# Kernel optimization log

Hardware: AMD Instinct MI355X
Metric: run time of the kernel (lower is better)

The kernel has to match this reference:

```python
import jax, jax.numpy as jnp
import numpy as np

QUERY_DIM, FEAT_DIM, HID_DIM, OUT_DIM = 512, 2048, 512, 512
B, L, S, T = 8, 128, 100, 100


def setup_inputs() -> dict:
    key = jax.random.key(0)
    ks = jax.random.split(key, 9)
    d = {
        "query": jax.random.normal(ks[0], (B, L, QUERY_DIM), jnp.float32),
        "src": jax.random.normal(ks[1], (B, S, FEAT_DIM), jnp.float32),
        "trg": jax.random.normal(ks[2], (B, T, FEAT_DIM), jnp.float32),
        # params (LinearAct == Linear + identity act); src/trg projections share weights
        "Wq": jax.random.normal(ks[3], (QUERY_DIM, HID_DIM), jnp.float32) / np.sqrt(QUERY_DIM),
        "bq": jnp.zeros((HID_DIM,), jnp.float32),
        "Ws": jax.random.normal(ks[4], (FEAT_DIM, HID_DIM), jnp.float32) / np.sqrt(FEAT_DIM),
        "bs": jnp.zeros((HID_DIM,), jnp.float32),
        "Wo": jax.random.normal(ks[5], (HID_DIM + QUERY_DIM, OUT_DIM), jnp.float32) / np.sqrt(HID_DIM + QUERY_DIM),
        "bo": jnp.zeros((OUT_DIM,), jnp.float32),
    }
    return d


def reference(query, src, trg, Wq, bq, Ws, bs, Wo, bo):
    b, l, _ = query.shape
    s = src.shape[1]
    t = trg.shape[1]
    q = query @ Wq + bq          # b,l,k
    s_key = src @ Ws + bs        # b,s,k
    t_key = trg @ Ws + bs        # b,t,k
    hid = q.shape[-1]
    # score[b,l,s,t] = q . (s_key - t_key)/sqrt(2) / sqrt(hid) -- decomposed, no b,s,t,k tensor
    qs = jnp.einsum('blk,bsk->bls', q, s_key)
    qt = jnp.einsum('blk,btk->blt', q, t_key)
    score = (qs[:, :, :, None] - qt[:, :, None, :]) / jnp.sqrt(jnp.asarray(2.0 * hid, q.dtype))
    w = jax.nn.softmax(score.reshape(b, l, s * t), axis=-1).reshape(b, l, s, t)
    # ctx = sum_{s,t} w * (s_key - t_key)/sqrt(2), decomposed via marginals
    ws = w.sum(axis=3)           # b,l,s
    wt = w.sum(axis=2)           # b,l,t
    ctx = (jnp.einsum('bls,bsk->blk', ws, s_key) - jnp.einsum('blt,btk->blk', wt, t_key)) / jnp.sqrt(jnp.asarray(2.0, q.dtype))
    x = jnp.concatenate([query, ctx], axis=-1) @ Wo + bo
    return x
```

## Files before the change

kernel.cpp:

```cpp
#include <hip/hip_runtime.h>
#include <math.h>


typedef __attribute__((ext_vector_type(8))) short s16x8;
typedef __attribute__((ext_vector_type(4))) float f32x4;

__device__ __forceinline__ unsigned short f2bf(float f) {
    unsigned int u = __float_as_uint(f);
    return (unsigned short)((u + 0x7fffu + ((u >> 16) & 1u)) >> 16);
}

__global__ __launch_bounds__(256) void k_prep(
    const float* __restrict__ query, const float* __restrict__ src,
    const float* __restrict__ trg, const float* __restrict__ Wq,
    const float* __restrict__ Ws, const float* __restrict__ Wo,
    const float* __restrict__ bs, unsigned short* __restrict__ qbf,
    unsigned short* __restrict__ aout, unsigned short* __restrict__ abf,
    unsigned short* __restrict__ WqT, unsigned short* __restrict__ WsT,
    unsigned short* __restrict__ WoT, float* __restrict__ keys) {
    __shared__ float tile[32][33];
    const int bid = blockIdx.x, t = threadIdx.x;

    if (bid < 3712) {
        const int idx = bid * 256 + t;
        if (idx < 131072) {
            float4 v = *(const float4*)(query + (size_t)idx * 4);
            ushort4 o = make_ushort4(f2bf(v.x), f2bf(v.y), f2bf(v.z), f2bf(v.w));
            *(ushort4*)(qbf + (size_t)idx * 4) = o;
            const int flat = idx * 4, m = flat >> 9, c = flat & 511;
            *(ushort4*)(aout + (size_t)m * 1024 + c) = o;
        } else if (idx < 540672) {
            const int i = idx - 131072;
            float4 v = *(const float4*)(src + (size_t)i * 4);
            *(ushort4*)(abf + (size_t)i * 4) =
                make_ushort4(f2bf(v.x), f2bf(v.y), f2bf(v.z), f2bf(v.w));
        } else {
            const int i = idx - 540672;
            float4 v = *(const float4*)(trg + (size_t)i * 4);
            *(ushort4*)(abf + 1638400 + (size_t)i * 4) =
                make_ushort4(f2bf(v.x), f2bf(v.y), f2bf(v.z), f2bf(v.w));
        }
    } else if (bid < 5504) {
        const int id = bid - 3712;
        const float* W; unsigned short* O; int K, tk, tn;
        if (id < 256)       { W = Wq; O = WqT; K = 512;  tk = id >> 4;          tn = id & 15; }
        else if (id < 1280) { W = Ws; O = WsT; K = 2048; tk = (id - 256) >> 4;  tn = (id - 256) & 15; }
        else                { W = Wo; O = WoT; K = 1024; tk = (id - 1280) >> 4; tn = (id - 1280) & 15; }
        const int row = t >> 3, c4 = (t & 7) * 4;
        float4 v = *(const float4*)(W + (size_t)(tk * 32 + row) * 512 + tn * 32 + c4);
        tile[row][c4 + 0] = v.x; tile[row][c4 + 1] = v.y;
        tile[row][c4 + 2] = v.z; tile[row][c4 + 3] = v.w;
        __syncthreads();
        ushort4 o = make_ushort4(f2bf(tile[c4 + 0][row]), f2bf(tile[c4 + 1][row]),
                                 f2bf(tile[c4 + 2][row]), f2bf(tile[c4 + 3][row]));
        *(ushort4*)(O + (size_t)(tn * 32 + row) * K + tk * 32 + c4) = o;
    } else {
        const int i = (bid - 5504) * 256 + t;
        const int f = i * 4;
        *(float4*)(keys + f) = *(const float4*)(bs + (f & 511));
    }
}


__device__ __forceinline__ void gemm64_atomic(
    const unsigned short* __restrict__ A, const unsigned short* __restrict__ BT,
    float* __restrict__ C, int m0, int n0, int K, int N, int kbase, int kiters,
    unsigned short* As, unsigned short* Bs) {
    const int t = threadIdx.x;
    const int lane = t & 63, wid = t >> 6;
    const int wm = (wid & 1) * 32, wn = (wid >> 1) * 32;
    const int lr = lane & 15, lq = lane >> 4;

    f32x4 acc[2][2] = {};
    for (int it = 0; it < kiters; it++) {
        const int kt = kbase + it * 64;
        __syncthreads();
#pragma unroll
        for (int i = 0; i < 2; i++) {
            const int idx = i * 256 + t, r = idx >> 3, c = idx & 7;
            *(s16x8*)&As[r * 72 + c * 8] =
                *(const s16x8*)(A + (size_t)(m0 + r) * K + kt + c * 8);
            *(s16x8*)&Bs[r * 72 + c * 8] =
                *(const s16x8*)(BT + (size_t)(n0 + r) * K + kt + c * 8);
        }
        __syncthreads();
#pragma unroll
        for (int s = 0; s < 2; s++) {
            s16x8 a0 = *(const s16x8*)&As[(wm + lr) * 72      + s * 32 + lq * 8];
            s16x8 a1 = *(const s16x8*)&As[(wm + 16 + lr) * 72 + s * 32 + lq * 8];
            s16x8 b0 = *(const s16x8*)&Bs[(wn + lr) * 72      + s * 32 + lq * 8];
            s16x8 b1 = *(const s16x8*)&Bs[(wn + 16 + lr) * 72 + s * 32 + lq * 8];
            acc[0][0] = __builtin_amdgcn_mfma_f32_16x16x32_bf16(a0, b0, acc[0][0], 0, 0, 0);
            acc[0][1] = __builtin_amdgcn_mfma_f32_16x16x32_bf16(a0, b1, acc[0][1], 0, 0, 0);
            acc[1][0] = __builtin_amdgcn_mfma_f32_16x16x32_bf16(a1, b0, acc[1][0], 0, 0, 0);
            acc[1][1] = __builtin_amdgcn_mfma_f32_16x16x32_bf16(a1, b1, acc[1][1], 0, 0, 0);
        }
    }
#pragma unroll
    for (int i = 0; i < 2; i++)
#pragma unroll
        for (int j = 0; j < 2; j++) {
            const int col = n0 + wn + j * 16 + lr;
            const int row = m0 + wm + i * 16 + lq * 4;
#pragma unroll
            for (int r = 0; r < 4; r++)
                unsafeAtomicAdd(&C[(size_t)(row + r) * N + col], acc[i][j][r]);
        }
}

__device__ __forceinline__ void gemm32(
    const unsigned short* __restrict__ A, const unsigned short* __restrict__ BT,
    const float* __restrict__ bias, float* __restrict__ C,
    int m0, int n0, int K, int N, int kiters,
    unsigned short* As, unsigned short* Bs) {
    const int t = threadIdx.x;
    const int lane = t & 63, wid = t >> 6;
    const int wm = (wid & 1) * 16, wn = (wid >> 1) * 32;
    const int lr = lane & 15, lq = lane >> 4;

    f32x4 acc[2] = {};
    for (int it = 0; it < kiters; it++) {
        const int kt = it * 64;
        __syncthreads();
        {
            const int r = t >> 3, c = t & 7;
            *(s16x8*)&As[r * 72 + c * 8] =
                *(const s16x8*)(A + (size_t)(m0 + r) * K + kt + c * 8);
        }
#pragma unroll
        for (int i = 0; i < 2; i++) {
            const int idx = i * 256 + t, r = idx >> 3, c = idx & 7;
            *(s16x8*)&Bs[r * 72 + c * 8] =
                *(const s16x8*)(BT + (size_t)(n0 + r) * K + kt + c * 8);
        }
        __syncthreads();
#pragma unroll
        for (int s = 0; s < 2; s++) {
            s16x8 a0 = *(const s16x8*)&As[(wm + lr) * 72      + s * 32 + lq * 8];
            s16x8 b0 = *(const s16x8*)&Bs[(wn + lr) * 72      + s * 32 + lq * 8];
            s16x8 b1 = *(const s16x8*)&Bs[(wn + 16 + lr) * 72 + s * 32 + lq * 8];
            acc[0] = __builtin_amdgcn_mfma_f32_16x16x32_bf16(a0, b0, acc[0], 0, 0, 0);
            acc[1] = __builtin_amdgcn_mfma_f32_16x16x32_bf16(a0, b1, acc[1], 0, 0, 0);
        }
    }
#pragma unroll
    for (int j = 0; j < 2; j++) {
        const int col = n0 + wn + j * 16 + lr;
        const int row = m0 + wm + lq * 4;
        const float bv = bias[col];
#pragma unroll
        for (int r = 0; r < 4; r++)
            C[(size_t)(row + r) * N + col] = acc[j][r] + bv;
    }
}

__global__ __launch_bounds__(256) void k_stageB(
    const unsigned short* __restrict__ qbf, const unsigned short* __restrict__ abf,
    const unsigned short* __restrict__ WqT, const unsigned short* __restrict__ WsT,
    const float* __restrict__ bq, float* __restrict__ q, float* __restrict__ keys) {
    __shared__ __align__(16) unsigned short As[64 * 72];
    __shared__ __align__(16) unsigned short Bs[64 * 72];
    const int bid = blockIdx.x;
    if (bid < 800) {
        const int c = bid / 200, rem = bid % 200;
        const int mt = rem >> 3, nt = rem & 7;
        gemm64_atomic(abf, WsT, keys, mt * 64, nt * 64, 2048, 512, c * 512, 8, As, Bs);
    } else {
        const int r = bid - 800;
        const int mt = r >> 3, nt = r & 7;
        gemm32(qbf, WqT, bq, q, mt * 32, nt * 64, 512, 512, 8, As, Bs);
    }
}

__global__ __launch_bounds__(256) void k_out(
    const unsigned short* __restrict__ aout, const unsigned short* __restrict__ WoT,
    const float* __restrict__ bo, float* __restrict__ out) {
    __shared__ __align__(16) unsigned short As[64 * 72];
    __shared__ __align__(16) unsigned short Bs[64 * 72];
    gemm32(aout, WoT, bo, out, blockIdx.y * 32, blockIdx.x * 64, 1024, 512, 16, As, Bs);
}

__global__ __launch_bounds__(256) void k_scores(
    const float* __restrict__ q, const float* __restrict__ keys,
    float* __restrict__ wsT, float* __restrict__ wtT) {
    __shared__ __align__(16) float qsh[512];
    __shared__ float sc[200];

    const int t = threadIdx.x;
    const int row = blockIdx.x;
    const int b = row >> 7, l = row & 127;

    if (t < 128)
        *(float4*)&qsh[t * 4] = *(const float4*)(q + (size_t)row * 512 + t * 4);
    __syncthreads();

    const int wave = t >> 6, lane = t & 63;
    const float4* qp = (const float4*)qsh;
    const float4 qv1 = qp[lane], qv2 = qp[lane + 64];

    for (int idx = wave; idx < 200; idx += 4) {
        const int kr = (idx < 100) ? (b * 100 + idx)
                                   : (800 + b * 100 + (idx - 100));
        const float4* kp = (const float4*)(keys + (size_t)kr * 512);
        const float4 kv1 = kp[lane], kv2 = kp[lane + 64];
        float d = kv1.x * qv1.x + kv1.y * qv1.y + kv1.z * qv1.z + kv1.w * qv1.w
                + kv2.x * qv2.x + kv2.y * qv2.y + kv2.z * qv2.z + kv2.w * qv2.w;
#pragma unroll
        for (int off = 32; off > 0; off >>= 1) d += __shfl_down(d, off);
        if (lane == 0)
            sc[idx] = ((idx < 100) ? d : -d) * (1.0f / 32.0f);
    }
    __syncthreads();

    if (wave < 2) {
        const float* sp = sc + wave * 100;
        const bool hi = (lane + 64) < 100;
        const float v0 = sp[lane];
        const float v1 = hi ? sp[lane + 64] : -INFINITY;
        float mx = fmaxf(v0, v1);
#pragma unroll
        for (int off = 32; off > 0; off >>= 1) mx = fmaxf(mx, __shfl_xor(mx, off));
        const float e0 = __expf(v0 - mx);
        const float e1 = hi ? __expf(v1 - mx) : 0.f;
        float s = e0 + e1;
#pragma unroll
        for (int off = 32; off > 0; off >>= 1) s += __shfl_xor(s, off);
        const float inv = 1.f / s;
        float* op = (wave == 0) ? wsT : wtT;
        op[(b * 100 + lane) * 128 + l] = e0 * inv;
        if (hi) op[(b * 100 + lane + 64) * 128 + l] = e1 * inv;
    }
}

__global__ __launch_bounds__(256) void k_ctx(
    const float* __restrict__ wsT, const float* __restrict__ wtT,
    const float* __restrict__ keys, unsigned short* __restrict__ aout) {
    __shared__ float As[40][64];
    __shared__ float Bs[40][32];

    const int t = threadIdx.x;
    const int b = blockIdx.y;
    const int n0 = blockIdx.x * 32;
    const int l0 = blockIdx.z * 64;
    const int tx = t & 7, ty = t >> 3;

    float acc[2][4] = {};

    for (int c5 = 0; c5 < 5; c5++) {
        const int kbase = c5 * 40;
        __syncthreads();
#pragma unroll
        for (int e = 0; e < 10; e++) {
            const int idx = t + e * 256;
            const int k = idx >> 6, j = idx & 63;
            const int kk = kbase + k;
            As[k][j] = (kk < 100) ? wsT[(b * 100 + kk) * 128 + l0 + j]
                                  : wtT[(b * 100 + (kk - 100)) * 128 + l0 + j];
        }
#pragma unroll
        for (int e = 0; e < 5; e++) {
            const int idx = t + e * 256;
            const int k = idx >> 5, j = idx & 31;
            const int kk = kbase + k;
            Bs[k][j] = (kk < 100)
                ?  keys[(size_t)(b * 100 + kk) * 512 + n0 + j]
                : -keys[(size_t)(800 + b * 100 + (kk - 100)) * 512 + n0 + j];
        }
        __syncthreads();
#pragma unroll 8
        for (int k = 0; k < 40; k++) {
            float ar0 = As[k][ty * 2], ar1 = As[k][ty * 2 + 1];
            float br[4];
            *(float4*)br = *(const float4*)&Bs[k][tx * 4];
#pragma unroll
            for (int j = 0; j < 4; j++) {
                acc[0][j] = fmaf(ar0, br[j], acc[0][j]);
                acc[1][j] = fmaf(ar1, br[j], acc[1][j]);
            }
        }
    }

    const float s2 = 0.70710678118654752f;
#pragma unroll
    for (int i = 0; i < 2; i++) {
        const int m = b * 128 + l0 + ty * 2 + i;
        ushort4 o = make_ushort4(f2bf(acc[i][0] * s2), f2bf(acc[i][1] * s2),
                                 f2bf(acc[i][2] * s2), f2bf(acc[i][3] * s2));
        *(ushort4*)(aout + (size_t)m * 1024 + 512 + n0 + tx * 4) = o;
    }
}


extern "C" void kernel_launch(void* const* d_in, const int* in_sizes, int n_in,
                              void* d_out, int out_size, void* d_ws, size_t ws_size,
                              hipStream_t stream) {
    const float* query = (const float*)d_in[0];
    const float* src   = (const float*)d_in[1];
    const float* trg   = (const float*)d_in[2];
    const float* Wq    = (const float*)d_in[3];
    const float* bq    = (const float*)d_in[4];
    const float* Ws    = (const float*)d_in[5];
    const float* bs    = (const float*)d_in[6];
    const float* Wo    = (const float*)d_in[7];
    const float* bo    = (const float*)d_in[8];
    float* out = (float*)d_out;

    float* q    = (float*)d_ws;
    float* keys = q    + 524288;
    float* wsT  = keys + 819200;
    float* wtT  = wsT  + 102400;
    unsigned short* qbf = (unsigned short*)(wtT + 102400);
    unsigned short* abf = qbf + 524288;
    unsigned short* aout= abf + 3276800;
    unsigned short* wqt = aout + 1048576;
    unsigned short* wst = wqt  + 262144;
    unsigned short* wot = wst  + 1048576;

    k_prep<<<6304, 256, 0, stream>>>(query, src, trg, Wq, Ws, Wo, bs,
                                     qbf, aout, abf, wqt, wst, wot, keys);
    k_stageB<<<1056, 256, 0, stream>>>(qbf, abf, wqt, wst, bq, q, keys);
    k_scores<<<1024, 256, 0, stream>>>(q, keys, wsT, wtT);
    k_ctx<<<dim3(16, 8, 2), 256, 0, stream>>>(wsT, wtT, keys, aout);
    k_out<<<dim3(8, 32), 256, 0, stream>>>(aout, wot, bo, out);
}
```

Baseline: 158.8 us.

## Fuse all stages into one persistent kernel with grid-wide barriers

Replaces the five separate kernel launches with one persistent kernel of 512 blocks that loops over virtual blocks for each stage. Stages are separated by software grid barriers built on an atomic counter, which is reset by a memset before each launch. The output GEMM now splits K in two and accumulates atomically into an output buffer pre-filled with the bias. The aim is to remove launch gaps and tail effects between stages. In exchange it relies on every block being co-resident, adds spin-wait barrier cost, and adds contention from the atomic accumulation.

```diff
diff --git a/kernel.cpp b/kernel.cpp
--- a/kernel.cpp
+++ b/kernel.cpp
@@ -4,63 +4,33 @@
 
 typedef __attribute__((ext_vector_type(8))) short s16x8;
 typedef __attribute__((ext_vector_type(4))) float f32x4;
+
+#define NBLK 512u
 
 __device__ __forceinline__ unsigned short f2bf(float f) {
     unsigned int u = __float_as_uint(f);
     return (unsigned short)((u + 0x7fffu + ((u >> 16) & 1u)) >> 16);
 }
 
-__global__ __launch_bounds__(256) void k_prep(
-    const float* __restrict__ query, const float* __restrict__ src,
-    const float* __restrict__ trg, const float* __restrict__ Wq,
-    const float* __restrict__ Ws, const float* __restrict__ Wo,
-    const float* __restrict__ bs, unsigned short* __restrict__ qbf,
-    unsigned short* __restrict__ aout, unsigned short* __restrict__ abf,
-    unsigned short* __restrict__ WqT, unsigned short* __restrict__ WsT,
-    unsigned short* __restrict__ WoT, float* __restrict__ keys) {
-    __shared__ float tile[32][33];
-    const int bid = blockIdx.x, t = threadIdx.x;
-
-    if (bid < 3712) {
-        const int idx = bid * 256 + t;
-        if (idx < 131072) {
-            float4 v = *(const float4*)(query + (size_t)idx * 4);
-            ushort4 o = make_ushort4(f2bf(v.x), f2bf(v.y), f2bf(v.z), f2bf(v.w));
-            *(ushort4*)(qbf + (size_t)idx * 4) = o;
-            const int flat = idx * 4, m = flat >> 9, c = flat & 511;
-            *(ushort4*)(aout + (size_t)m * 1024 + c) = o;
-        } else if (idx < 540672) {
-            const int i = idx - 131072;
-            float4 v = *(const float4*)(src + (size_t)i * 4);
-            *(ushort4*)(abf + (size_t)i * 4) =
-                make_ushort4(f2bf(v.x), f2bf(v.y), f2bf(v.z), f2bf(v.w));
-        } else {
-            const int i = idx - 540672;
-            float4 v = *(const float4*)(trg + (size_t)i * 4);
-            *(ushort4*)(abf + 1638400 + (size_t)i * 4) =
-                make_ushort4(f2bf(v.x), f2bf(v.y), f2bf(v.z), f2bf(v.w));
-        }
-    } else if (bid < 5504) {
-        const int id = bid - 3712;
-        const float* W; unsigned short* O; int K, tk, tn;
-        if (id < 256)       { W = Wq; O = WqT; K = 512;  tk = id >> 4;          tn = id & 15; }
-        else if (id < 1280) { W = Ws; O = WsT; K = 2048; tk = (id - 256) >> 4;  tn = (id - 256) & 15; }
-        else                { W = Wo; O = WoT; K = 1024; tk = (id - 1280) >> 4; tn = (id - 1280) & 15; }
-        const int row = t >> 3, c4 = (t & 7) * 4;
-        float4 v = *(const float4*)(W + (size_t)(tk * 32 + row) * 512 + tn * 32 + c4);
-        tile[row][c4 + 0] = v.x; tile[row][c4 + 1] = v.y;
-        tile[row][c4 + 2] = v.z; tile[row][c4 + 3] = v.w;
-        __syncthreads();
-        ushort4 o = make_ushort4(f2bf(tile[c4 + 0][row]), f2bf(tile[c4 + 1][row]),
-                                 f2bf(tile[c4 + 2][row]), f2bf(tile[c4 + 3][row]));
-        *(ushort4*)(O + (size_t)(tn * 32 + row) * K + tk * 32 + c4) = o;
-    } else {
-        const int i = (bid - 5504) * 256 + t;
-        const int f = i * 4;
-        *(float4*)(keys + f) = *(const float4*)(bs + (f & 511));
-    }
-}
-
+__device__ __forceinline__ void gbar(unsigned* cnt) {
+    __syncthreads();
+    if (threadIdx.x == 0) {
+        __hip_atomic_fetch_add(cnt, 1u, __ATOMIC_RELEASE,
+                               __HIP_MEMORY_SCOPE_AGENT);
+        unsigned spins = 0;
+        while (__hip_atomic_load(cnt, __ATOMIC_ACQUIRE,
+                                 __HIP_MEMORY_SCOPE_AGENT) < NBLK &&
+               ++spins < (8u << 20)) { }
+    }
+    __syncthreads();
+}
+
+struct MegaArgs {
+    const float *query, *src, *trg, *Wq, *bq, *Ws, *bs, *Wo, *bo;
+    unsigned short *qbf, *abf, *aout, *wqt, *wst, *wot;
+    float *q, *keys, *wsT, *wtT, *out;
+    unsigned *bar;
+};
 
 __device__ __forceinline__ void gemm64_atomic(
     const unsigned short* __restrict__ A, const unsigned short* __restrict__ BT,
@@ -108,10 +78,11 @@
         }
 }
 
+template <bool ATOMIC>
 __device__ __forceinline__ void gemm32(
     const unsigned short* __restrict__ A, const unsigned short* __restrict__ BT,
     const float* __restrict__ bias, float* __restrict__ C,
-    int m0, int n0, int K, int N, int kiters,
+    int m0, int n0, int K, int N, int kbase, int kiters,
     unsigned short* As, unsigned short* Bs) {
     const int t = threadIdx.x;
     const int lane = t & 63, wid = t >> 6;
@@ -120,7 +91,7 @@
 
     f32x4 acc[2] = {};
     for (int it = 0; it < kiters; it++) {
-        const int kt = it * 64;
+        const int kt = kbase + it * 64;
         __syncthreads();
         {
             const int r = t >> 3, c = t & 7;
@@ -147,163 +118,215 @@
     for (int j = 0; j < 2; j++) {
         const int col = n0 + wn + j * 16 + lr;
         const int row = m0 + wm + lq * 4;
-        const float bv = bias[col];
-#pragma unroll
-        for (int r = 0; r < 4; r++)
-            C[(size_t)(row + r) * N + col] = acc[j][r] + bv;
-    }
-}
-
-__global__ __launch_bounds__(256) void k_stageB(
-    const unsigned short* __restrict__ qbf, const unsigned short* __restrict__ abf,
-    const unsigned short* __restrict__ WqT, const unsigned short* __restrict__ WsT,
-    const float* __restrict__ bq, float* __restrict__ q, float* __restrict__ keys) {
-    __shared__ __align__(16) unsigned short As[64 * 72];
-    __shared__ __align__(16) unsigned short Bs[64 * 72];
-    const int bid = blockIdx.x;
-    if (bid < 800) {
-        const int c = bid / 200, rem = bid % 200;
+        if (ATOMIC) {
+#pragma unroll
+            for (int r = 0; r < 4; r++)
+                unsafeAtomicAdd(&C[(size_t)(row + r) * N + col], acc[j][r]);
+        } else {
+            const float bv = bias[col];
+#pragma unroll
+            for (int r = 0; r < 4; r++)
+                C[(size_t)(row + r) * N + col] = acc[j][r] + bv;
+        }
+    }
+}
+
+__global__ __launch_bounds__(256, 2) void k_mega(MegaArgs p) {
+    __shared__ __align__(16) unsigned char smem[18432];
+    unsigned short* As = (unsigned short*)smem;
+    unsigned short* Bs = (unsigned short*)(smem + 9216);
+    const int t = threadIdx.x;
+    const int nb = gridDim.x;
+
+    for (int vb = blockIdx.x; vb < 6816; vb += nb) {
+        if (vb < 3712) {
+            const int idx = vb * 256 + t;
+            if (idx < 131072) {
+                float4 v = *(const float4*)(p.query + (size_t)idx * 4);
+                ushort4 o = make_ushort4(f2bf(v.x), f2bf(v.y), f2bf(v.z), f2bf(v.w));
+                *(ushort4*)(p.qbf + (size_t)idx * 4) = o;
+                const int flat = idx * 4, m = flat >> 9, c = flat & 511;
+                *(ushort4*)(p.aout + (size_t)m * 1024 + c) = o;
+            } else if (idx < 540672) {
+                const int i = idx - 131072;
+                float4 v = *(const float4*)(p.src + (size_t)i * 4);
+                *(ushort4*)(p.abf + (size_t)i * 4) =
+                    make_ushort4(f2bf(v.x), f2bf(v.y), f2bf(v.z), f2bf(v.w));
+            } else {
+                const int i = idx - 540672;
+                float4 v = *(const float4*)(p.trg + (size_t)i * 4);
+                *(ushort4*)(p.abf + 1638400 + (size_t)i * 4) =
+                    make_ushort4(f2bf(v.x), f2bf(v.y), f2bf(v.z), f2bf(v.w));
+            }
+        } else if (vb < 5504) {
+            float* tile = (float*)smem;
+            const int id = vb - 3712;
+            const float* W; unsigned short* O; int K, tk, tn;
+            if (id < 256)       { W = p.Wq; O = p.wqt; K = 512;  tk = id >> 4;          tn = id & 15; }
+            else if (id < 1280) { W = p.Ws; O = p.wst; K = 2048; tk = (id - 256) >> 4;  tn = (id - 256) & 15; }
+            else                { W = p.Wo; O = p.wot; K = 1024; tk = (id - 1280) >> 4; tn = (id - 1280) & 15; }
+            const int row = t >> 3, c4 = (t & 7) * 4;
+            float4 v = *(const float4*)(W + (size_t)(tk * 32 + row) * 512 + tn * 32 + c4);
+            tile[row * 33 + c4 + 0] = v.x; tile[row * 33 + c4 + 1] = v.y;
+            tile[row * 33 + c4 + 2] = v.z; tile[row * 33 + c4 + 3] = v.w;
+            __syncthreads();
+            ushort4 o = make_ushort4(
+                f2bf(tile[(c4 + 0) * 33 + row]), f2bf(tile[(c4 + 1) * 33 + row]),
+                f2bf(tile[(c4 + 2) * 33 + row]), f2bf(tile[(c4 + 3) * 33 + row]));
+            *(ushort4*)(O + (size_t)(tn * 32 + row) * K + tk * 32 + c4) = o;
+            __syncthreads();
+        } else if (vb < 6304) {
+            const int f = ((vb - 5504) * 256 + t) * 4;
+            *(float4*)(p.keys + f) = *(const float4*)(p.bs + (f & 511));
+        } else {
+            const int f = ((vb - 6304) * 256 + t) * 4;
+            *(float4*)(p.out + f) = *(const float4*)(p.bo + (f & 511));
+        }
+    }
+    gbar(p.bar + 0);
+
+    for (int vb = blockIdx.x; vb < 1056; vb += nb) {
+        if (vb < 800) {
+            const int c = vb / 200, rem = vb % 200;
+            const int mt = rem >> 3, nt = rem & 7;
+            gemm64_atomic(p.abf, p.wst, p.keys, mt * 64, nt * 64, 2048, 512,
+                          c * 512, 8, As, Bs);
+        } else {
+            const int r = vb - 800;
+            const int mt = r >> 3, nt = r & 7;
+            gemm32<false>(p.qbf, p.wqt, p.bq, p.q, mt * 32, nt * 64, 512, 512,
+                          0, 8, As, Bs);
+        }
+    }
+    gbar(p.bar + 16);
+
+    {
+        float* qsh = (float*)smem;
+        float* sc  = (float*)(smem + 2048);
+        const int wave = t >> 6, lane = t & 63;
+        for (int vb = blockIdx.x; vb < 1024; vb += nb) {
+            const int b = vb >> 7, l = vb & 127;
+            if (t < 128)
+                *(float4*)&qsh[t * 4] =
+                    *(const float4*)(p.q + (size_t)vb * 512 + t * 4);
+            __syncthreads();
+            const float4* qp = (const float4*)qsh;
+            const float4 qv1 = qp[lane], qv2 = qp[lane + 64];
+
+            for (int idx = wave; idx < 200; idx += 4) {
+                const int kr = (idx < 100) ? (b * 100 + idx)
+                                           : (800 + b * 100 + (idx - 100));
+                const float4* kp = (const float4*)(p.keys + (size_t)kr * 512);
+                const float4 kv1 = kp[lane], kv2 = kp[lane + 64];
+                float d = kv1.x * qv1.x + kv1.y * qv1.y + kv1.z * qv1.z + kv1.w * qv1.w
+                        + kv2.x * qv2.x + kv2.y * qv2.y + kv2.z * qv2.z + kv2.w * qv2.w;
+#pragma unroll
+                for (int off = 32; off > 0; off >>= 1) d += __shfl_down(d, off);
+                if (lane == 0)
+                    sc[idx] = ((idx < 100) ? d : -d) * (1.0f / 32.0f);
+            }
+            __syncthreads();
+
+            if (wave < 2) {
+                const float* sp = sc + wave * 100;
+                const bool hi = (lane + 64) < 100;
+                const float v0 = sp[lane];
+                const float v1 = hi ? sp[lane + 64] : -INFINITY;
+                float mx = fmaxf(v0, v1);
+#pragma unroll
+                for (int off = 32; off > 0; off >>= 1) mx = fmaxf(mx, __shfl_xor(mx, off));
+                const float e0 = __expf(v0 - mx);
+                const float e1 = hi ? __expf(v1 - mx) : 0.f;
+                float s = e0 + e1;
+#pragma unroll
+                for (int off = 32; off > 0; off >>= 1) s += __shfl_xor(s, off);
+                const float inv = 1.f / s;
+                float* op = (wave == 0) ? p.wsT : p.wtT;
+                op[(b * 100 + lane) * 128 + l] = e0 * inv;
+                if (hi) op[(b * 100 + lane + 64) * 128 + l] = e1 * inv;
+            }
+            __syncthreads();
+        }
+    }
+    gbar(p.bar + 32);
+
+    {
+        float* cAs = (float*)smem;
+        float* cBs = (float*)(smem + 10240);
+        const int tx = t & 7, ty = t >> 3;
+        for (int vb = blockIdx.x; vb < 256; vb += nb) {
+            const int n0 = (vb & 15) * 32;
+            const int b  = (vb >> 4) & 7;
+            const int l0 = (vb >> 7) * 64;
+            float acc[2][4] = {};
+            for (int c5 = 0; c5 < 5; c5++) {
+                const int kbase = c5 * 40;
+                __syncthreads();
+#pragma unroll
+                for (int e = 0; e < 10; e++) {
+                    const int idx = t + e * 256;
+                    const int k = idx >> 6, j = idx & 63;
+                    const int kk = kbase + k;
+                    cAs[k * 64 + j] = (kk < 100)
+                        ? p.wsT[(b * 100 + kk) * 128 + l0 + j]
+                        : p.wtT[(b * 100 + (kk - 100)) * 128 + l0 + j];
+                }
+#pragma unroll
+                for (int e = 0; e < 5; e++) {
+                    const int idx = t + e * 256;
+                    const int k = idx >> 5, j = idx & 31;
+                    const int kk = kbase + k;
+                    cBs[k * 32 + j] = (kk < 100)
+                        ?  p.keys[(size_t)(b * 100 + kk) * 512 + n0 + j]
+                        : -p.keys[(size_t)(800 + b * 100 + (kk - 100)) * 512 + n0 + j];
+                }
+                __syncthreads();
+#pragma unroll 8
+                for (int k = 0; k < 40; k++) {
+                    float ar0 = cAs[k * 64 + ty * 2], ar1 = cAs[k * 64 + ty * 2 + 1];
+                    float br[4];
+                    *(float4*)br = *(const float4*)&cBs[k * 32 + tx * 4];
+#pragma unroll
+                    for (int j = 0; j < 4; j++) {
+                        acc[0][j] = fmaf(ar0, br[j], acc[0][j]);
+                        acc[1][j] = fmaf(ar1, br[j], acc[1][j]);
+                    }
+                }
+            }
+            const float s2 = 0.70710678118654752f;
+#pragma unroll
+            for (int i = 0; i < 2; i++) {
+                const int m = b * 128 + l0 + ty * 2 + i;
+                ushort4 o = make_ushort4(f2bf(acc[i][0] * s2), f2bf(acc[i][1] * s2),
+                                         f2bf(acc[i][2] * s2), f2bf(acc[i][3] * s2));
+                *(ushort4*)(p.aout + (size_t)m * 1024 + 512 + n0 + tx * 4) = o;
+            }
+        }
+    }
+    gbar(p.bar + 48);
+
+    for (int vb = blockIdx.x; vb < 512; vb += nb) {
+        const int c = vb >> 8, rem = vb & 255;
         const int mt = rem >> 3, nt = rem & 7;
-        gemm64_atomic(abf, WsT, keys, mt * 64, nt * 64, 2048, 512, c * 512, 8, As, Bs);
-    } else {
-        const int r = bid - 800;
-        const int mt = r >> 3, nt = r & 7;
-        gemm32(qbf, WqT, bq, q, mt * 32, nt * 64, 512, 512, 8, As, Bs);
-    }
-}
-
-__global__ __launch_bounds__(256) void k_out(
-    const unsigned short* __restrict__ aout, const unsigned short* __restrict__ WoT,
-    const float* __restrict__ bo, float* __restrict__ out) {
-    __shared__ __align__(16) unsigned short As[64 * 72];
-    __shared__ __align__(16) unsigned short Bs[64 * 72];
-    gemm32(aout, WoT, bo, out, blockIdx.y * 32, blockIdx.x * 64, 1024, 512, 16, As, Bs);
-}
-
-__global__ __launch_bounds__(256) void k_scores(
-    const float* __restrict__ q, const float* __restrict__ keys,
-    float* __restrict__ wsT, float* __restrict__ wtT) {
-    __shared__ __align__(16) float qsh[512];
-    __shared__ float sc[200];
-
-    const int t = threadIdx.x;
-    const int row = blockIdx.x;
-    const int b = row >> 7, l = row & 127;
-
-    if (t < 128)
-        *(float4*)&qsh[t * 4] = *(const float4*)(q + (size_t)row * 512 + t * 4);
-    __syncthreads();
-
-    const int wave = t >> 6, lane = t & 63;
-    const float4* qp = (const float4*)qsh;
-    const float4 qv1 = qp[lane], qv2 = qp[lane + 64];
-
-    for (int idx = wave; idx < 200; idx += 4) {
-        const int kr = (idx < 100) ? (b * 100 + idx)
-                                   : (800 + b * 100 + (idx - 100));
-        const float4* kp = (const float4*)(keys + (size_t)kr * 512);
-        const float4 kv1 = kp[lane], kv2 = kp[lane + 64];
-        float d = kv1.x * qv1.x + kv1.y * qv1.y + kv1.z * qv1.z + kv1.w * qv1.w
-                + kv2.x * qv2.x + kv2.y * qv2.y + kv2.z * qv2.z + kv2.w * qv2.w;
-#pragma unroll
-        for (int off = 32; off > 0; off >>= 1) d += __shfl_down(d, off);
-        if (lane == 0)
-            sc[idx] = ((idx < 100) ? d : -d) * (1.0f / 32.0f);
-    }
-    __syncthreads();
-
-    if (wave < 2) {
-        const float* sp = sc + wave * 100;
-        const bool hi = (lane + 64) < 100;
-        const float v0 = sp[lane];
-        const float v1 = hi ? sp[lane + 64] : -INFINITY;
-        float mx = fmaxf(v0, v1);
-#pragma unroll
-        for (int off = 32; off > 0; off >>= 1) mx = fmaxf(mx, __shfl_xor(mx, off));
-        const float e0 = __expf(v0 - mx);
-        const float e1 = hi ? __expf(v1 - mx) : 0.f;
-        float s = e0 + e1;
-#pragma unroll
-        for (int off = 32; off > 0; off >>= 1) s += __shfl_xor(s, off);
-        const float inv = 1.f / s;
-        float* op = (wave == 0) ? wsT : wtT;
-        op[(b * 100 + lane) * 128 + l] = e0 * inv;
-        if (hi) op[(b * 100 + lane + 64) * 128 + l] = e1 * inv;
-    }
-}
-
-__global__ __launch_bounds__(256) void k_ctx(
-    const float* __restrict__ wsT, const float* __restrict__ wtT,
-    const float* __restrict__ keys, unsigned short* __restrict__ aout) {
-    __shared__ float As[40][64];
-    __shared__ float Bs[40][32];
-
-    const int t = threadIdx.x;
-    const int b = blockIdx.y;
-    const int n0 = blockIdx.x * 32;
-    const int l0 = blockIdx.z * 64;
-    const int tx = t & 7, ty = t >> 3;
-
-    float acc[2][4] = {};
-
-    for (int c5 = 0; c5 < 5; c5++) {
-        const int kbase = c5 * 40;
-        __syncthreads();
-#pragma unroll
-        for (int e = 0; e < 10; e++) {
-            const int idx = t + e * 256;
-            const int k = idx >> 6, j = idx & 63;
-            const int kk = kbase + k;
-            As[k][j] = (kk < 100) ? wsT[(b * 100 + kk) * 128 + l0 + j]
-                                  : wtT[(b * 100 + (kk - 100)) * 128 + l0 + j];
-        }
-#pragma unroll
-        for (int e = 0; e < 5; e++) {
-            const int idx = t + e * 256;
-            const int k = idx >> 5, j = idx & 31;
-            const int kk = kbase + k;
-            Bs[k][j] = (kk < 100)
-                ?  keys[(size_t)(b * 100 + kk) * 512 + n0 + j]
-                : -keys[(size_t)(800 + b * 100 + (kk - 100)) * 512 + n0 + j];
-        }
-        __syncthreads();
-#pragma unroll 8
-        for (int k = 0; k < 40; k++) {
-            float ar0 = As[k][ty * 2], ar1 = As[k][ty * 2 + 1];
-            float br[4];
-            *(float4*)br = *(const float4*)&Bs[k][tx * 4];
-#pragma unroll
-            for (int j = 0; j < 4; j++) {
-                acc[0][j] = fmaf(ar0, br[j], acc[0][j]);
-                acc[1][j] = fmaf(ar1, br[j], acc[1][j]);
-            }
-        }
-    }
-
-    const float s2 = 0.70710678118654752f;
-#pragma unroll
-    for (int i = 0; i < 2; i++) {
-        const int m = b * 128 + l0 + ty * 2 + i;
-        ushort4 o = make_ushort4(f2bf(acc[i][0] * s2), f2bf(acc[i][1] * s2),
-                                 f2bf(acc[i][2] * s2), f2bf(acc[i][3] * s2));
-        *(ushort4*)(aout + (size_t)m * 1024 + 512 + n0 + tx * 4) = o;
-    }
-}
-
+        gemm32<true>(p.aout, p.wot, nullptr, p.out, mt * 32, nt * 64, 1024, 512,
+                     c * 512, 8, As, Bs);
+    }
+}
 
 extern "C" void kernel_launch(void* const* d_in, const int* in_sizes, int n_in,
                               void* d_out, int out_size, void* d_ws, size_t ws_size,
                               hipStream_t stream) {
-    const float* query = (const float*)d_in[0];
-    const float* src   = (const float*)d_in[1];
-    const float* trg   = (const float*)d_in[2];
-    const float* Wq    = (const float*)d_in[3];
-    const float* bq    = (const float*)d_in[4];
-    const float* Ws    = (const float*)d_in[5];
-    const float* bs    = (const float*)d_in[6];
-    const float* Wo    = (const float*)d_in[7];
-    const float* bo    = (const float*)d_in[8];
-    float* out = (float*)d_out;
+    MegaArgs a;
+    a.query = (const float*)d_in[0];
+    a.src   = (const float*)d_in[1];
+    a.trg   = (const float*)d_in[2];
+    a.Wq    = (const float*)d_in[3];
+    a.bq    = (const float*)d_in[4];
+    a.Ws    = (const float*)d_in[5];
+    a.bs    = (const float*)d_in[6];
+    a.Wo    = (const float*)d_in[7];
+    a.bo    = (const float*)d_in[8];
+    a.out   = (float*)d_out;
 
     float* q    = (float*)d_ws;
     float* keys = q    + 524288;
@@ -315,11 +338,13 @@
     unsigned short* wqt = aout + 1048576;
     unsigned short* wst = wqt  + 262144;
     unsigned short* wot = wst  + 1048576;
-
-    k_prep<<<6304, 256, 0, stream>>>(query, src, trg, Wq, Ws, Wo, bs,
-                                     qbf, aout, abf, wqt, wst, wot, keys);
-    k_stageB<<<1056, 256, 0, stream>>>(qbf, abf, wqt, wst, bq, q, keys);
-    k_scores<<<1024, 256, 0, stream>>>(q, keys, wsT, wtT);
-    k_ctx<<<dim3(16, 8, 2), 256, 0, stream>>>(wsT, wtT, keys, aout);
-    k_out<<<dim3(8, 32), 256, 0, stream>>>(aout, wot, bo, out);
-}
+    unsigned* bar = (unsigned*)(wot + 524288);
+
+    a.q = q; a.keys = keys; a.wsT = wsT; a.wtT = wtT;
+    a.qbf = qbf; a.abf = abf; a.aout = aout;
+    a.wqt = wqt; a.wst = wst; a.wot = wot;
+    a.bar = bar;
+
+    hipMemsetAsync(bar, 0, 256, stream);
+    k_mega<<<dim3(NBLK), dim3(256), 0, stream>>>(a);
+}
```

Measured after the change: 394.2 us. 148% more time.

## Prefetch GEMM tiles into registers, split-K output GEMM, and shrink ctx tiles

Applied to the files above, without the earlier changes.

The GEMM helpers now load the next K tile into registers while the current tile is being computed from LDS, a register-level double buffer that hides global latency. The output GEMM is split along K into two halves that accumulate atomically into an output pre-filled with the bias by the prep kernel. The ctx kernel uses 32-row tiles with register prefetch, so it launches twice as many blocks. These changes raise parallelism and overlap at the cost of atomics, extra register pressure, and a bias pre-fill pass over the output.

```diff
diff --git a/kernel.cpp b/kernel.cpp
--- a/kernel.cpp
+++ b/kernel.cpp
@@ -14,10 +14,11 @@
     const float* __restrict__ query, const float* __restrict__ src,
     const float* __restrict__ trg, const float* __restrict__ Wq,
     const float* __restrict__ Ws, const float* __restrict__ Wo,
-    const float* __restrict__ bs, unsigned short* __restrict__ qbf,
-    unsigned short* __restrict__ aout, unsigned short* __restrict__ abf,
-    unsigned short* __restrict__ WqT, unsigned short* __restrict__ WsT,
-    unsigned short* __restrict__ WoT, float* __restrict__ keys) {
+    const float* __restrict__ bs, const float* __restrict__ bo,
+    unsigned short* __restrict__ qbf, unsigned short* __restrict__ aout,
+    unsigned short* __restrict__ abf, unsigned short* __restrict__ WqT,
+    unsigned short* __restrict__ WsT, unsigned short* __restrict__ WoT,
+    float* __restrict__ keys, float* __restrict__ out) {
     __shared__ float tile[32][33];
     const int bid = blockIdx.x, t = threadIdx.x;
 
@@ -54,10 +55,12 @@
         ushort4 o = make_ushort4(f2bf(tile[c4 + 0][row]), f2bf(tile[c4 + 1][row]),
                                  f2bf(tile[c4 + 2][row]), f2bf(tile[c4 + 3][row]));
         *(ushort4*)(O + (size_t)(tn * 32 + row) * K + tk * 32 + c4) = o;
+    } else if (bid < 6304) {
+        const int f = ((bid - 5504) * 256 + t) * 4;
+        *(float4*)(keys + f) = *(const float4*)(bs + (f & 511));
     } else {
-        const int i = (bid - 5504) * 256 + t;
-        const int f = i * 4;
-        *(float4*)(keys + f) = *(const float4*)(bs + (f & 511));
+        const int f = ((bid - 6304) * 256 + t) * 4;
+        *(float4*)(out + f) = *(const float4*)(bo + (f & 511));
     }
 }
 
@@ -70,20 +73,25 @@
     const int lane = t & 63, wid = t >> 6;
     const int wm = (wid & 1) * 32, wn = (wid >> 1) * 32;
     const int lr = lane & 15, lq = lane >> 4;
+    const int r = t >> 3, c8 = (t & 7) * 8;
+
+    s16x8 ra0, ra1, rb0, rb1;
+#define LD64(kt)                                                           \
+    ra0 = *(const s16x8*)(A  + (size_t)(m0 + r)      * K + (kt) + c8);     \
+    ra1 = *(const s16x8*)(A  + (size_t)(m0 + r + 32) * K + (kt) + c8);     \
+    rb0 = *(const s16x8*)(BT + (size_t)(n0 + r)      * K + (kt) + c8);     \
+    rb1 = *(const s16x8*)(BT + (size_t)(n0 + r + 32) * K + (kt) + c8);
 
     f32x4 acc[2][2] = {};
+    LD64(kbase);
     for (int it = 0; it < kiters; it++) {
-        const int kt = kbase + it * 64;
-        __syncthreads();
-#pragma unroll
-        for (int i = 0; i < 2; i++) {
-            const int idx = i * 256 + t, r = idx >> 3, c = idx & 7;
-            *(s16x8*)&As[r * 72 + c * 8] =
-                *(const s16x8*)(A + (size_t)(m0 + r) * K + kt + c * 8);
-            *(s16x8*)&Bs[r * 72 + c * 8] =
-                *(const s16x8*)(BT + (size_t)(n0 + r) * K + kt + c * 8);
-        }
-        __syncthreads();
+        __syncthreads();
+        *(s16x8*)&As[r * 72 + c8]        = ra0;
+        *(s16x8*)&As[(r + 32) * 72 + c8] = ra1;
+        *(s16x8*)&Bs[r * 72 + c8]        = rb0;
+        *(s16x8*)&Bs[(r + 32) * 72 + c8] = rb1;
+        __syncthreads();
+        if (it + 1 < kiters) { LD64(kbase + (it + 1) * 64); }
 #pragma unroll
         for (int s = 0; s < 2; s++) {
             s16x8 a0 = *(const s16x8*)&As[(wm + lr) * 72      + s * 32 + lq * 8];
@@ -96,6 +104,7 @@
             acc[1][1] = __builtin_amdgcn_mfma_f32_16x16x32_bf16(a1, b1, acc[1][1], 0, 0, 0);
         }
     }
+#undef LD64
 #pragma unroll
     for (int i = 0; i < 2; i++)
 #pragma unroll
@@ -103,37 +112,38 @@
             const int col = n0 + wn + j * 16 + lr;
             const int row = m0 + wm + i * 16 + lq * 4;
 #pragma unroll
-            for (int r = 0; r < 4; r++)
-                unsafeAtomicAdd(&C[(size_t)(row + r) * N + col], acc[i][j][r]);
-        }
-}
-
+            for (int rr = 0; rr < 4; rr++)
+                unsafeAtomicAdd(&C[(size_t)(row + rr) * N + col], acc[i][j][rr]);
+        }
+}
+
+template <bool ATOMIC>
 __device__ __forceinline__ void gemm32(
     const unsigned short* __restrict__ A, const unsigned short* __restrict__ BT,
     const float* __restrict__ bias, float* __restrict__ C,
-    int m0, int n0, int K, int N, int kiters,
+    int m0, int n0, int K, int N, int kbase, int kiters,
     unsigned short* As, unsigned short* Bs) {
     const int t = threadIdx.x;
     const int lane = t & 63, wid = t >> 6;
     const int wm = (wid & 1) * 16, wn = (wid >> 1) * 32;
     const int lr = lane & 15, lq = lane >> 4;
+    const int r = t >> 3, c8 = (t & 7) * 8;
+
+    s16x8 ra, rb0, rb1;
+#define LD32(kt)                                                           \
+    ra  = *(const s16x8*)(A  + (size_t)(m0 + r)      * K + (kt) + c8);     \
+    rb0 = *(const s16x8*)(BT + (size_t)(n0 + r)      * K + (kt) + c8);     \
+    rb1 = *(const s16x8*)(BT + (size_t)(n0 + r + 32) * K + (kt) + c8);
 
     f32x4 acc[2] = {};
+    LD32(kbase);
     for (int it = 0; it < kiters; it++) {
-        const int kt = it * 64;
-        __syncthreads();
-        {
-            const int r = t >> 3, c = t & 7;
-            *(s16x8*)&As[r * 72 + c * 8] =
-                *(const s16x8*)(A + (size_t)(m0 + r) * K + kt + c * 8);
-        }
-#pragma unroll
-        for (int i = 0; i < 2; i++) {
-            const int idx = i * 256 + t, r = idx >> 3, c = idx & 7;
-            *(s16x8*)&Bs[r * 72 + c * 8] =
-                *(const s16x8*)(BT + (size_t)(n0 + r) * K + kt + c * 8);
-        }
-        __syncthreads();
+        __syncthreads();
+        *(s16x8*)&As[r * 72 + c8]        = ra;
+        *(s16x8*)&Bs[r * 72 + c8]        = rb0;
+        *(s16x8*)&Bs[(r + 32) * 72 + c8] = rb1;
+        __syncthreads();
+        if (it + 1 < kiters) { LD32(kbase + (it + 1) * 64); }
 #pragma unroll
         for (int s = 0; s < 2; s++) {
             s16x8 a0 = *(const s16x8*)&As[(wm + lr) * 72      + s * 32 + lq * 8];
@@ -143,14 +153,21 @@
             acc[1] = __builtin_amdgcn_mfma_f32_16x16x32_bf16(a0, b1, acc[1], 0, 0, 0);
         }
     }
+#undef LD32
 #pragma unroll
     for (int j = 0; j < 2; j++) {
         const int col = n0 + wn + j * 16 + lr;
         const int row = m0 + wm + lq * 4;
-        const float bv = bias[col];
-#pragma unroll
-        for (int r = 0; r < 4; r++)
-            C[(size_t)(row + r) * N + col] = acc[j][r] + bv;
+        if (ATOMIC) {
+#pragma unroll
+            for (int rr = 0; rr < 4; rr++)
+                unsafeAtomicAdd(&C[(size_t)(row + rr) * N + col], acc[j][rr]);
+        } else {
+            const float bv = bias[col];
+#pragma unroll
+            for (int rr = 0; rr < 4; rr++)
+                C[(size_t)(row + rr) * N + col] = acc[j][rr] + bv;
+        }
     }
 }
 
@@ -168,16 +185,20 @@
     } else {
         const int r = bid - 800;
         const int mt = r >> 3, nt = r & 7;
-        gemm32(qbf, WqT, bq, q, mt * 32, nt * 64, 512, 512, 8, As, Bs);
+        gemm32<false>(qbf, WqT, bq, q, mt * 32, nt * 64, 512, 512, 0, 8, As, Bs);
     }
 }
 
 __global__ __launch_bounds__(256) void k_out(
     const unsigned short* __restrict__ aout, const unsigned short* __restrict__ WoT,
-    const float* __restrict__ bo, float* __restrict__ out) {
+    float* __restrict__ out) {
     __shared__ __align__(16) unsigned short As[64 * 72];
     __shared__ __align__(16) unsigned short Bs[64 * 72];
-    gemm32(aout, WoT, bo, out, blockIdx.y * 32, blockIdx.x * 64, 1024, 512, 16, As, Bs);
+    const int bid = blockIdx.x;
+    const int c = bid >> 8, rem = bid & 255;
+    const int mt = rem >> 3, nt = rem & 7;
+    gemm32<true>(aout, WoT, nullptr, out, mt * 32, nt * 64, 1024, 512,
+                 c * 512, 8, As, Bs);
 }
 
 __global__ __launch_bounds__(256) void k_scores(
@@ -235,59 +256,57 @@
 __global__ __launch_bounds__(256) void k_ctx(
     const float* __restrict__ wsT, const float* __restrict__ wtT,
     const float* __restrict__ keys, unsigned short* __restrict__ aout) {
-    __shared__ float As[40][64];
+    __shared__ float As[40][32];
     __shared__ float Bs[40][32];
 
     const int t = threadIdx.x;
     const int b = blockIdx.y;
     const int n0 = blockIdx.x * 32;
-    const int l0 = blockIdx.z * 64;
+    const int l0 = blockIdx.z * 32;
     const int tx = t & 7, ty = t >> 3;
 
-    float acc[2][4] = {};
-
-    for (int c5 = 0; c5 < 5; c5++) {
-        const int kbase = c5 * 40;
-        __syncthreads();
-#pragma unroll
-        for (int e = 0; e < 10; e++) {
-            const int idx = t + e * 256;
-            const int k = idx >> 6, j = idx & 63;
-            const int kk = kbase + k;
-            As[k][j] = (kk < 100) ? wsT[(b * 100 + kk) * 128 + l0 + j]
-                                  : wtT[(b * 100 + (kk - 100)) * 128 + l0 + j];
-        }
+    float rA[5], rB[5];
+    auto loadc = [&](int kbase) {
 #pragma unroll
         for (int e = 0; e < 5; e++) {
             const int idx = t + e * 256;
             const int k = idx >> 5, j = idx & 31;
             const int kk = kbase + k;
-            Bs[k][j] = (kk < 100)
+            rA[e] = (kk < 100) ? wsT[(b * 100 + kk) * 128 + l0 + j]
+                               : wtT[(b * 100 + (kk - 100)) * 128 + l0 + j];
+            rB[e] = (kk < 100)
                 ?  keys[(size_t)(b * 100 + kk) * 512 + n0 + j]
                 : -keys[(size_t)(800 + b * 100 + (kk - 100)) * 512 + n0 + j];
         }
-        __syncthreads();
+    };
+
+    float acc[4] = {};
+    loadc(0);
+    for (int c5 = 0; c5 < 5; c5++) {
+        __syncthreads();
+#pragma unroll
+        for (int e = 0; e < 5; e++) {
+            const int idx = t + e * 256;
+            As[idx >> 5][idx & 31] = rA[e];
+            Bs[idx >> 5][idx & 31] = rB[e];
+        }
+        __syncthreads();
+        if (c5 < 4) loadc((c5 + 1) * 40);
 #pragma unroll 8
         for (int k = 0; k < 40; k++) {
-            float ar0 = As[k][ty * 2], ar1 = As[k][ty * 2 + 1];
+            const float ar = As[k][ty];
             float br[4];
             *(float4*)br = *(const float4*)&Bs[k][tx * 4];
 #pragma unroll
-            for (int j = 0; j < 4; j++) {
-                acc[0][j] = fmaf(ar0, br[j], acc[0][j]);
-                acc[1][j] = fmaf(ar1, br[j], acc[1][j]);
-            }
+            for (int j = 0; j < 4; j++) acc[j] = fmaf(ar, br[j], acc[j]);
         }
     }
 
     const float s2 = 0.70710678118654752f;
-#pragma unroll
-    for (int i = 0; i < 2; i++) {
-        const int m = b * 128 + l0 + ty * 2 + i;
-        ushort4 o = make_ushort4(f2bf(acc[i][0] * s2), f2bf(acc[i][1] * s2),
-                                 f2bf(acc[i][2] * s2), f2bf(acc[i][3] * s2));
-        *(ushort4*)(aout + (size_t)m * 1024 + 512 + n0 + tx * 4) = o;
-    }
+    const int m = b * 128 + l0 + ty;
+    ushort4 o = make_ushort4(f2bf(acc[0] * s2), f2bf(acc[1] * s2),
+                             f2bf(acc[2] * s2), f2bf(acc[3] * s2));
+    *(ushort4*)(aout + (size_t)m * 1024 + 512 + n0 + tx * 4) = o;
 }
 
 
@@ -316,10 +335,10 @@
     unsigned short* wst = wqt  + 262144;
     unsigned short* wot = wst  + 1048576;
 
-    k_prep<<<6304, 256, 0, stream>>>(query, src, trg, Wq, Ws, Wo, bs,
-                                     qbf, aout, abf, wqt, wst, wot, keys);
+    k_prep<<<6816, 256, 0, stream>>>(query, src, trg, Wq, Ws, Wo, bs, bo,
+                                     qbf, aout, abf, wqt, wst, wot, keys, out);
     k_stageB<<<1056, 256, 0, stream>>>(qbf, abf, wqt, wst, bq, q, keys);
     k_scores<<<1024, 256, 0, stream>>>(q, keys, wsT, wtT);
-    k_ctx<<<dim3(16, 8, 2), 256, 0, stream>>>(wsT, wtT, keys, aout);
-    k_out<<<dim3(8, 32), 256, 0, stream>>>(aout, wot, bo, out);
-}
+    k_ctx<<<dim3(16, 8, 4), 256, 0, stream>>>(wsT, wtT, keys, aout);
+    k_out<<<512, 256, 0, stream>>>(aout, wot, out);
+}
```

Result: faster. 150.4 us (-5.3%).
